# Kernel optimization log

Hardware: AMD Instinct MI355X
Metric: run time of the kernel (lower is better)

Reference implementation:

```python
import jax, jax.numpy as jnp
import numpy as np

B, M, K, N = 4, 2048, 4096, 4096


def setup_inputs() -> dict:
    key = jax.random.key(0)
    k1, k2, k3, k4, k5 = jax.random.split(key, 5)
    # quantized activations in [-8, 7], stored as int8 (spec dtype int32, cast here)
    x_q = jax.random.randint(k1, (B, M, K), -8, 8, dtype=jnp.int32).astype(jnp.int8)
    # per-token activation scales (B, M, 1)
    scales_x = jax.random.uniform(k2, (B, M, 1), dtype=jnp.float32, minval=0.001, maxval=0.02)
    # int8 weight (N, K) in [-8, 7] as produced by from_float
    weight = jax.random.randint(k3, (N, K), -8, 8, dtype=jnp.int32).astype(jnp.int8)
    # per-output-row weight scales (N, 1)
    weight_scales = jax.random.uniform(k4, (N, 1), dtype=jnp.float32, minval=0.001, maxval=0.02)
    bias = jax.random.normal(k5, (N,), dtype=jnp.float32) * 0.02
    return {"x_q": x_q, "scales_x": scales_x, "weight": weight,
            "weight_scales": weight_scales, "bias": bias}


def reference(x_q, scales_x, weight, weight_scales, bias):
    acc = jnp.einsum('bmk,nk->bmn', x_q, weight,
                     preferred_element_type=jnp.int32)  # (B, M, N) int32
    # sym_dequant: per-token scale * per-row weight scale, then fused bias add
    out = acc.astype(jnp.float32) * scales_x * weight_scales.reshape(1, 1, N) + bias
    return out
```

## Files before the change

kernel.cpp:

```cpp
#include <hip/hip_runtime.h>
#include <stdint.h>

#define MROWS 8192
#define K_DIM 4096
#define N_DIM 4096
#define BM 256
#define BN 256
#define BK 64
#define KT (K_DIM / BK)
#define ABYTES (BM * BK)
#define TBYTES (2 * ABYTES)

#define X_ELEMS (MROWS * K_DIM)
#define W_ELEMS (N_DIM * K_DIM)

typedef __attribute__((ext_vector_type(4))) int   int4v;
typedef __attribute__((ext_vector_type(4))) float float4v;

#define GLOAD_LDS16(gptr, lptr)                                                   \
    __builtin_amdgcn_global_load_lds((const __attribute__((address_space(1))) void*)(gptr), \
                                     (__attribute__((address_space(3))) void*)(lptr), 16, 0, 0)

__device__ __forceinline__ int pack4(int4v v) {
    return (int)((unsigned)(v[0] & 0xFF)
               | ((unsigned)(v[1] & 0xFF) << 8)
               | ((unsigned)(v[2] & 0xFF) << 16)
               | ((unsigned)(v[3] & 0xFF) << 24));
}

__global__ __launch_bounds__(256) void pack_i32_to_i8(
    const int4v* __restrict__ srcX, int* __restrict__ dstX, int n4x,
    const int4v* __restrict__ srcW, int* __restrict__ dstW, int n4w)
{
    const int stride = gridDim.x * blockDim.x;
    const int n4 = n4x + n4w;
    for (int i = blockIdx.x * blockDim.x + threadIdx.x; i < n4; i += stride) {
        if (i < n4x) dstX[i] = pack4(srcX[i]);
        else         dstW[i - n4x] = pack4(srcW[i - n4x]);
    }
}


#define TILE_BODY(T, AC, BC, AN, BN_)                                          \
  {                                                                            \
    asm volatile("s_waitcnt vmcnt(4)" ::: "memory");                           \
    __builtin_amdgcn_s_barrier();                                              \
    __builtin_amdgcn_sched_barrier(0);                                         \
    const int u_ = ((T) + 3) & (KT - 1);                                       \
    const size_t ko_ = (size_t)u_ * BK;                                        \
    int8_t* nbb_ = lds8 + (((T) + 3) & 3) * TBYTES;                            \
    GLOAD_LDS16(gA0 + ko_, nbb_ + dA0);                                        \
    GLOAD_LDS16(gA1 + ko_, nbb_ + dA1);                                        \
    GLOAD_LDS16(gB0 + ko_, nbb_ + dB0);                                        \
    GLOAD_LDS16(gB1 + ko_, nbb_ + dB1);                                        \
    const int8_t* rb_ = lds8 + (((T) + 1) & 3) * TBYTES;                       \
    _Pragma("unroll") for (int i_ = 0; i_ < 8; ++i_)                           \
        AN[i_] = *(const int4v*)(rb_ + aoff + i_ * 1024);                      \
    _Pragma("unroll") for (int j_ = 0; j_ < 4; ++j_)                           \
        BN_[j_] = *(const int4v*)(rb_ + boff + j_ * 1024);                     \
    __builtin_amdgcn_sched_barrier(0);                                         \
    __builtin_amdgcn_s_setprio(1);                                             \
    _Pragma("unroll") for (int i_ = 0; i_ < 8; ++i_)                           \
      _Pragma("unroll") for (int j_ = 0; j_ < 4; ++j_)                         \
        acc[i_][j_] = __builtin_amdgcn_mfma_i32_16x16x64_i8(                   \
                          AC[i_], BC[j_], acc[i_][j_], 0, 0, 0);               \
    __builtin_amdgcn_s_setprio(0);                                             \
    __builtin_amdgcn_sched_barrier(0);                                         \
  }

__global__ __launch_bounds__(512, 2) void i8gemm_dq_kernel(
    const int8_t* __restrict__ xq,
    const float*  __restrict__ sx,
    const int8_t* __restrict__ wt,
    const float*  __restrict__ ws,
    const float*  __restrict__ bias,
    float*        __restrict__ out)
{
    __shared__ __align__(16) int8_t lds8[4 * TBYTES];

    const int tid  = threadIdx.x;
    const int wave = tid >> 6;
    const int lane = tid & 63;
    const int wr   = wave >> 2;
    const int wcn  = wave & 3;

    const int bid = blockIdx.x;
    const int wg  = (bid & 7) * 64 + (bid >> 3);
    const int ct  = wg & 15;
    const int rt  = wg >> 4;

    const int srow = wave * 16 + (lane >> 2);
    const int scol = (((lane & 3) - ((lane >> 3) & 3)) & 3) * 16;
    const int8_t* gA0 = xq + (size_t)(rt * BM + srow) * K_DIM + scol;
    const int8_t* gA1 = gA0 + (size_t)128 * K_DIM;
    const int8_t* gB0 = wt + (size_t)(ct * BN + srow) * K_DIM + scol;
    const int8_t* gB1 = gB0 + (size_t)128 * K_DIM;
    const int dA0 = wave * 1024;
    const int dA1 = 8192 + wave * 1024;
    const int dB0 = ABYTES + wave * 1024;
    const int dB1 = ABYTES + 8192 + wave * 1024;

    const int mrow = lane & 15;
    const int kswz = (((lane >> 4) + (mrow >> 1)) & 3) * 16;
    const int aoff = (wr * 128 + mrow) * BK + kswz;
    const int boff = ABYTES + (wcn * 64 + mrow) * BK + kswz;

    int4v acc[8][4] = {};

    #pragma unroll
    for (int u = 0; u < 3; ++u) {
        const size_t ko = (size_t)u * BK;
        int8_t* bb = lds8 + u * TBYTES;
        GLOAD_LDS16(gA0 + ko, bb + dA0);
        GLOAD_LDS16(gA1 + ko, bb + dA1);
        GLOAD_LDS16(gB0 + ko, bb + dB0);
        GLOAD_LDS16(gB1 + ko, bb + dB1);
    }

    int4v a0f[8], b0f[4], a1f[8], b1f[4];
    {
        asm volatile("s_waitcnt vmcnt(8)" ::: "memory");
        __builtin_amdgcn_s_barrier();
        __builtin_amdgcn_sched_barrier(0);
        const int8_t* rb = lds8;
        #pragma unroll
        for (int i = 0; i < 8; ++i) a0f[i] = *(const int4v*)(rb + aoff + i * 1024);
        #pragma unroll
        for (int j = 0; j < 4; ++j) b0f[j] = *(const int4v*)(rb + boff + j * 1024);
    }

    for (int tt = 0; tt < KT; tt += 2) {
        TILE_BODY(tt,     a0f, b0f, a1f, b1f);
        TILE_BODY(tt + 1, a1f, b1f, a0f, b0f);
    }

    asm volatile("s_waitcnt vmcnt(0)" ::: "memory");

    const int row_base = rt * BM + wr * 128;
    const int col_base = ct * BN + wcn * 64;
    const int crow = (lane >> 4) * 4;
    const int ccol = lane & 15;

    float wsc[4], bsc[4];
    #pragma unroll
    for (int j = 0; j < 4; ++j) {
        const int c = col_base + j * 16 + ccol;
        wsc[j] = ws[c];
        bsc[j] = bias[c];
    }

    #pragma unroll
    for (int i = 0; i < 8; ++i) {
        const int r0 = row_base + i * 16 + crow;
        const float4v sx4 = *(const float4v*)(sx + r0);
        #pragma unroll
        for (int j = 0; j < 4; ++j) {
            const int c = col_base + j * 16 + ccol;
            float* o = out + (size_t)r0 * N_DIM + c;
            #pragma unroll
            for (int r = 0; r < 4; ++r)
                o[(size_t)r * N_DIM] = (float)acc[i][j][r] * sx4[r] * wsc[j] + bsc[j];
        }
    }
}

extern "C" void kernel_launch(void* const* d_in, const int* in_sizes, int n_in,
                              void* d_out, int out_size, void* d_ws, size_t ws_size,
                              hipStream_t stream) {
    const int*   xq32 = (const int*)d_in[0];
    const float* sx   = (const float*)d_in[1];
    const int*   wt32 = (const int*)d_in[2];
    const float* ws   = (const float*)d_in[3];
    const float* bias = (const float*)d_in[4];
    float* out = (float*)d_out;

    int8_t* xq8 = (int8_t*)d_ws;
    int8_t* wt8 = xq8 + (size_t)X_ELEMS;

    {
        int n4x = X_ELEMS / 4;
        int n4w = W_ELEMS / 4;
        pack_i32_to_i8<<<2048, 256, 0, stream>>>((const int4v*)xq32, (int*)xq8, n4x,
                                                 (const int4v*)wt32, (int*)wt8, n4w);
    }

    dim3 grid((MROWS / BM) * (N_DIM / BN));
    i8gemm_dq_kernel<<<grid, 512, 0, stream>>>(xq8, sx, wt8, ws, bias, out);
}
```

Measured before the change: 392.7 us.

## Shrink GEMM tile to 256x128 with 3-stage LDS pipeline and higher occupancy

Reduces the block tile N dimension from 256 to 128 and splits the 8 waves as a 4x2 grid, each owning a 64x64 output subtile. The LDS ring drops from four to three slots, and the register-double-buffered fragment prefetch is replaced by a simpler load-then-compute step per tile. Launch bounds now ask for four blocks per SM instead of two. The smaller tile lowers register and LDS use to allow more resident waves, at the cost of less data reuse per block and no overlap of LDS reads with MFMA inside a wave.

```diff
diff --git a/kernel.cpp b/kernel.cpp
--- a/kernel.cpp
+++ b/kernel.cpp
@@ -5,11 +5,12 @@
 #define K_DIM 4096
 #define N_DIM 4096
 #define BM 256
-#define BN 256
+#define BN 128
 #define BK 64
 #define KT (K_DIM / BK)
-#define ABYTES (BM * BK)
-#define TBYTES (2 * ABYTES)
+#define A_BYTES (BM * BK)
+#define B_BYTES (BN * BK)
+#define SLOT (A_BYTES + B_BYTES)
 
 #define X_ELEMS (MROWS * K_DIM)
 #define W_ELEMS (N_DIM * K_DIM)
@@ -40,35 +41,7 @@
     }
 }
 
-
-#define TILE_BODY(T, AC, BC, AN, BN_)                                          \
-  {                                                                            \
-    asm volatile("s_waitcnt vmcnt(4)" ::: "memory");                           \
-    __builtin_amdgcn_s_barrier();                                              \
-    __builtin_amdgcn_sched_barrier(0);                                         \
-    const int u_ = ((T) + 3) & (KT - 1);                                       \
-    const size_t ko_ = (size_t)u_ * BK;                                        \
-    int8_t* nbb_ = lds8 + (((T) + 3) & 3) * TBYTES;                            \
-    GLOAD_LDS16(gA0 + ko_, nbb_ + dA0);                                        \
-    GLOAD_LDS16(gA1 + ko_, nbb_ + dA1);                                        \
-    GLOAD_LDS16(gB0 + ko_, nbb_ + dB0);                                        \
-    GLOAD_LDS16(gB1 + ko_, nbb_ + dB1);                                        \
-    const int8_t* rb_ = lds8 + (((T) + 1) & 3) * TBYTES;                       \
-    _Pragma("unroll") for (int i_ = 0; i_ < 8; ++i_)                           \
-        AN[i_] = *(const int4v*)(rb_ + aoff + i_ * 1024);                      \
-    _Pragma("unroll") for (int j_ = 0; j_ < 4; ++j_)                           \
-        BN_[j_] = *(const int4v*)(rb_ + boff + j_ * 1024);                     \
-    __builtin_amdgcn_sched_barrier(0);                                         \
-    __builtin_amdgcn_s_setprio(1);                                             \
-    _Pragma("unroll") for (int i_ = 0; i_ < 8; ++i_)                           \
-      _Pragma("unroll") for (int j_ = 0; j_ < 4; ++j_)                         \
-        acc[i_][j_] = __builtin_amdgcn_mfma_i32_16x16x64_i8(                   \
-                          AC[i_], BC[j_], acc[i_][j_], 0, 0, 0);               \
-    __builtin_amdgcn_s_setprio(0);                                             \
-    __builtin_amdgcn_sched_barrier(0);                                         \
-  }
-
-__global__ __launch_bounds__(512, 2) void i8gemm_dq_kernel(
+__global__ __launch_bounds__(512, 4) void i8gemm_dq_kernel(
     const int8_t* __restrict__ xq,
     const float*  __restrict__ sx,
     const int8_t* __restrict__ wt,
@@ -76,68 +49,85 @@
     const float*  __restrict__ bias,
     float*        __restrict__ out)
 {
-    __shared__ __align__(16) int8_t lds8[4 * TBYTES];
+    __shared__ __align__(16) int8_t lds8[3 * SLOT];
 
     const int tid  = threadIdx.x;
     const int wave = tid >> 6;
     const int lane = tid & 63;
-    const int wr   = wave >> 2;
-    const int wcn  = wave & 3;
+    const int wrow = wave >> 1;
+    const int wcol = wave & 1;
 
     const int bid = blockIdx.x;
-    const int wg  = (bid & 7) * 64 + (bid >> 3);
-    const int ct  = wg & 15;
-    const int rt  = wg >> 4;
+    const int wg  = (bid & 7) * 128 + (bid >> 3);
+    const int ct  = wg & 31;
+    const int rt  = wg >> 5;
 
     const int srow = wave * 16 + (lane >> 2);
     const int scol = (((lane & 3) - ((lane >> 3) & 3)) & 3) * 16;
     const int8_t* gA0 = xq + (size_t)(rt * BM + srow) * K_DIM + scol;
     const int8_t* gA1 = gA0 + (size_t)128 * K_DIM;
-    const int8_t* gB0 = wt + (size_t)(ct * BN + srow) * K_DIM + scol;
-    const int8_t* gB1 = gB0 + (size_t)128 * K_DIM;
+    const int8_t* gB  = wt + (size_t)(ct * BN + srow) * K_DIM + scol;
     const int dA0 = wave * 1024;
     const int dA1 = 8192 + wave * 1024;
-    const int dB0 = ABYTES + wave * 1024;
-    const int dB1 = ABYTES + 8192 + wave * 1024;
+    const int dB  = A_BYTES + wave * 1024;
 
     const int mrow = lane & 15;
     const int kswz = (((lane >> 4) + (mrow >> 1)) & 3) * 16;
-    const int aoff = (wr * 128 + mrow) * BK + kswz;
-    const int boff = ABYTES + (wcn * 64 + mrow) * BK + kswz;
+    const int aoff = (wrow * 64 + mrow) * BK + kswz;
+    const int boff = A_BYTES + (wcol * 64 + mrow) * BK + kswz;
 
-    int4v acc[8][4] = {};
+    int4v acc[4][4] = {};
 
-    #pragma unroll
-    for (int u = 0; u < 3; ++u) {
-        const size_t ko = (size_t)u * BK;
-        int8_t* bb = lds8 + u * TBYTES;
-        GLOAD_LDS16(gA0 + ko, bb + dA0);
-        GLOAD_LDS16(gA1 + ko, bb + dA1);
-        GLOAD_LDS16(gB0 + ko, bb + dB0);
-        GLOAD_LDS16(gB1 + ko, bb + dB1);
+#define STAGE(U, S)                                        \
+    {                                                      \
+        const size_t ko_ = (size_t)(U) * BK;               \
+        int8_t* bb_ = lds8 + (S) * SLOT;                   \
+        GLOAD_LDS16(gA0 + ko_, bb_ + dA0);                 \
+        GLOAD_LDS16(gA1 + ko_, bb_ + dA1);                 \
+        GLOAD_LDS16(gB  + ko_, bb_ + dB);                  \
     }
 
-    int4v a0f[8], b0f[4], a1f[8], b1f[4];
-    {
-        asm volatile("s_waitcnt vmcnt(8)" ::: "memory");
+#define COMPUTE(S)                                                             \
+    {                                                                          \
+        const int8_t* base_ = lds8 + (S) * SLOT;                               \
+        int4v a_[4], b_[4];                                                    \
+        _Pragma("unroll") for (int i_ = 0; i_ < 4; ++i_)                       \
+            a_[i_] = *(const int4v*)(base_ + aoff + i_ * 1024);                \
+        _Pragma("unroll") for (int j_ = 0; j_ < 4; ++j_)                       \
+            b_[j_] = *(const int4v*)(base_ + boff + j_ * 1024);                \
+        __builtin_amdgcn_s_setprio(1);                                         \
+        _Pragma("unroll") for (int i_ = 0; i_ < 4; ++i_)                       \
+          _Pragma("unroll") for (int j_ = 0; j_ < 4; ++j_)                     \
+            acc[i_][j_] = __builtin_amdgcn_mfma_i32_16x16x64_i8(               \
+                              a_[i_], b_[j_], acc[i_][j_], 0, 0, 0);           \
+        __builtin_amdgcn_s_setprio(0);                                         \
+    }
+
+    STAGE(0, 0);
+    STAGE(1, 1);
+
+    #pragma unroll 3
+    for (int t = 0; t < KT - 2; ++t) {
+        asm volatile("s_waitcnt vmcnt(3)" ::: "memory");
         __builtin_amdgcn_s_barrier();
         __builtin_amdgcn_sched_barrier(0);
-        const int8_t* rb = lds8;
-        #pragma unroll
-        for (int i = 0; i < 8; ++i) a0f[i] = *(const int4v*)(rb + aoff + i * 1024);
-        #pragma unroll
-        for (int j = 0; j < 4; ++j) b0f[j] = *(const int4v*)(rb + boff + j * 1024);
+        STAGE(t + 2, (t + 2) % 3);
+        COMPUTE(t % 3);
     }
+    asm volatile("s_waitcnt vmcnt(3)" ::: "memory");
+    __builtin_amdgcn_s_barrier();
+    __builtin_amdgcn_sched_barrier(0);
+    COMPUTE((KT - 2) % 3);
+    asm volatile("s_waitcnt vmcnt(0)" ::: "memory");
+    __builtin_amdgcn_s_barrier();
+    __builtin_amdgcn_sched_barrier(0);
+    COMPUTE((KT - 1) % 3);
 
-    for (int tt = 0; tt < KT; tt += 2) {
-        TILE_BODY(tt,     a0f, b0f, a1f, b1f);
-        TILE_BODY(tt + 1, a1f, b1f, a0f, b0f);
-    }
+#undef STAGE
+#undef COMPUTE
 
-    asm volatile("s_waitcnt vmcnt(0)" ::: "memory");
-
-    const int row_base = rt * BM + wr * 128;
-    const int col_base = ct * BN + wcn * 64;
+    const int row_base = rt * BM + wrow * 64;
+    const int col_base = ct * BN + wcol * 64;
     const int crow = (lane >> 4) * 4;
     const int ccol = lane & 15;
 
@@ -150,7 +140,7 @@
     }
 
     #pragma unroll
-    for (int i = 0; i < 8; ++i) {
+    for (int i = 0; i < 4; ++i) {
         const int r0 = row_base + i * 16 + crow;
         const float4v sx4 = *(const float4v*)(sx + r0);
         #pragma unroll
```

New measurement: 413.8 us. 1.05x slower.
